# Performance work log

Measured on AMD Instinct MI355X. Metric: run time of the kernel, lower is better.

The kernel has to match this reference:

```python
import jax, jax.numpy as jnp
import numpy as np

CUTOFF = 32.0  # matches init_kwargs cutoff


def _reduce_single(elem, cutoff):
    """elem: [T, D]. Returns (means_padded [T, D], n_segs scalar int32).

    Faithful to the torch loop: representative = elem[0]; walk frames; when
    ||rep - frame|| > cutoff, close the segment [rep_id:f_ind] (mean over it)
    and restart at `frame`. Final open segment is also emitted. Because the
    number of segments is data-dependent, we return a fixed-shape [T, D]
    buffer whose first n_segs rows are the stacked segment means (rest zeros).
    """
    T, D = elem.shape

    def step(rep, frame):
        d = jnp.linalg.norm(rep - frame)  # torch.norm default = Frobenius/L2
        new_seg = d > cutoff
        rep = jnp.where(new_seg, frame, rep)
        return rep, new_seg

    # flags[i] == True means frame i+1 starts a new segment
    _, flags = jax.lax.scan(step, elem[0], elem[1:])
    flags = jnp.concatenate([jnp.zeros((1,), dtype=bool), flags])  # frame 0 never starts anew
    seg_id = jnp.cumsum(flags.astype(jnp.int32))  # [T], ordered segment ids
    n_segs = seg_id[-1] + 1

    sums = jax.ops.segment_sum(elem, seg_id, num_segments=T)  # [T, D]
    counts = jax.ops.segment_sum(jnp.ones((T,), elem.dtype), seg_id, num_segments=T)  # [T]
    means = sums / jnp.maximum(counts, 1.0)[:, None]  # padded rows stay 0
    return means, n_segs


def setup_inputs() -> dict:
    key = jax.random.key(0)
    batch = jax.random.normal(key, (16, 4096, 512), dtype=jnp.float32)
    return {"batch": batch}


def reference(batch):
    # vmap over the list-of-sequences batch dim (all sequences same length T)
    means, n_segs = jax.vmap(lambda e: _reduce_single(e, CUTOFF))(batch)
    return means, n_segs
```

## Files before the change

### kernel.cpp

```cpp
#include <hip/hip_runtime.h>

#define NB 16
#define NT 4096
#define ND 512
#define NLEV 12
#define UPSTRIDE 4104

__global__ __launch_bounds__(256) void kA_next(const float* __restrict__ in,
                                               int* __restrict__ nxt) {
    int lin  = blockIdx.x * 4 + (threadIdx.x >> 6);
    int lane = threadIdx.x & 63;
    int b = lin >> 12;
    int j = lin & (NT - 1);
    const float* base = in + (size_t)b * NT * ND;
    const float4* repp = (const float4*)(base + (size_t)j * ND);
    float4 r0 = repp[lane];
    float4 r1 = repp[lane + 64];
    int i = j + 1;
    for (; i < NT; ++i) {
        const float4* fp = (const float4*)(base + (size_t)i * ND);
        float4 x0 = fp[lane];
        float4 x1 = fp[lane + 64];
        float d0 = r0.x - x0.x, d1 = r0.y - x0.y, d2 = r0.z - x0.z, d3 = r0.w - x0.w;
        float d4 = r1.x - x1.x, d5 = r1.y - x1.y, d6 = r1.z - x1.z, d7 = r1.w - x1.w;
        double s = (double)d0 * d0 + (double)d1 * d1 + (double)d2 * d2 + (double)d3 * d3
                 + (double)d4 * d4 + (double)d5 * d5 + (double)d6 * d6 + (double)d7 * d7;
        #pragma unroll
        for (int off = 32; off >= 1; off >>= 1) s += __shfl_xor(s, off, 64);
        float sf = (float)s;
        if (sqrtf(sf) > 32.0f) break;
    }
    if (lane == 0) nxt[b * NT + j] = i;
}

__global__ __launch_bounds__(256) void kB_build(const int* __restrict__ nxt,
                                                unsigned short* __restrict__ up) {
    __shared__ unsigned short cur[NT + 8];
    __shared__ unsigned short nx[NT + 8];
    int b = blockIdx.x;
    int t = threadIdx.x;
    for (int j = t; j <= NT; j += 256)
        cur[j] = (j < NT) ? (unsigned short)nxt[b * NT + j] : (unsigned short)NT;
    __syncthreads();
    {
        unsigned short* d0 = up + (size_t)(0 * NB + b) * UPSTRIDE;
        for (int j = t; j <= NT; j += 256) d0[j] = cur[j];
    }
    for (int k = 1; k < NLEV; ++k) {
        for (int j = t; j <= NT; j += 256) nx[j] = cur[cur[j]];
        __syncthreads();
        for (int j = t; j <= NT; j += 256) cur[j] = nx[j];
        __syncthreads();
        unsigned short* dk = up + (size_t)(k * NB + b) * UPSTRIDE;
        for (int j = t; j <= NT; j += 256) dk[j] = cur[j];
    }
}

__global__ __launch_bounds__(256) void kC_descend(const unsigned short* __restrict__ up,
                                                  int* __restrict__ start,
                                                  int* __restrict__ nseg,
                                                  float* __restrict__ out_tail) {
    int idx = blockIdx.x * 256 + threadIdx.x;
    int b = idx >> 12;
    int i = idx & (NT - 1);
    int pos = 0, cnt = 0;
    #pragma unroll
    for (int k = NLEV - 1; k >= 0; --k) {
        int t = up[(size_t)(k * NB + b) * UPSTRIDE + pos];
        if (t <= i) { pos = t; cnt += (1 << k); }
    }
    if (pos == i) start[b * NT + cnt] = i;
    if (i == NT - 1) {
        nseg[b] = cnt + 1;
        out_tail[b] = (float)(cnt + 1);
    }
}

__global__ __launch_bounds__(128) void kD_means(const float* __restrict__ in,
                                                const int* __restrict__ nxt,
                                                const int* __restrict__ start,
                                                const int* __restrict__ nseg,
                                                float* __restrict__ out) {
    int r = blockIdx.x & (NT - 1);
    int b = blockIdx.x >> 12;
    int t = threadIdx.x;
    float4 acc = make_float4(0.f, 0.f, 0.f, 0.f);
    int n = nseg[b];
    if (r < n) {
        int s = start[b * NT + r];
        int e = nxt[b * NT + s];
        const float4* base = (const float4*)(in + (size_t)(b * NT + s) * ND);
        int cnt = e - s;
        for (int f = 0; f < cnt; ++f) {
            float4 v = base[(size_t)f * (ND / 4) + t];
            acc.x += v.x; acc.y += v.y; acc.z += v.z; acc.w += v.w;
        }
        float c = (float)cnt;
        acc.x /= c; acc.y /= c; acc.z /= c; acc.w /= c;
    }
    ((float4*)out)[(size_t)(b * NT + r) * (ND / 4) + t] = acc;
}

extern "C" void kernel_launch(void* const* d_in, const int* in_sizes, int n_in,
                              void* d_out, int out_size, void* d_ws, size_t ws_size,
                              hipStream_t stream) {
    const float* in = (const float*)d_in[0];
    float* out = (float*)d_out;
    char* ws = (char*)d_ws;

    int*            nxt   = (int*)(ws + 0);
    int*            start = (int*)(ws + 262144);
    int*            nseg  = (int*)(ws + 524288);
    unsigned short* up    = (unsigned short*)(ws + 524352);

    kA_next   <<<NB * NT / 4,  256, 0, stream>>>(in, nxt);
    kB_build  <<<NB,           256, 0, stream>>>(nxt, up);
    kC_descend<<<NB * NT / 256,256, 0, stream>>>(up, start, nseg,
                                                 out + (size_t)NB * NT * ND);
    kD_means  <<<NB * NT,      128, 0, stream>>>(in, nxt, start, nseg, out);
}
```

Measured before the change: 363.9 us.

## Screen distances in fp32 with exact fallback, unroll scan by four, retile builds

The next-segment search now computes four candidate rows at once using fp32 FMAs and interleaved wave reductions. Only rows whose squared distance falls near the threshold are recomputed with the original double-precision path, which removes most fp64 work and serialized shuffle chains. The pointer-jumping build kernel moves to 1024 threads per block. The means kernel assigns eight output rows per wave with 256-thread blocks, so far fewer blocks are launched. The screening band assumes fp32 error stays below 0.25, which risks mismatches if that bound is violated.

```diff
diff --git a/kernel.cpp b/kernel.cpp
--- a/kernel.cpp
+++ b/kernel.cpp
@@ -5,6 +5,46 @@
 #define ND 512
 #define NLEV 12
 #define UPSTRIDE 4104
+
+#define DIST8_F32(sout, y0, y1)                                   \
+    {                                                             \
+        float d_;                                                 \
+        d_ = r0.x - (y0).x; sout = d_ * d_;                       \
+        d_ = r0.y - (y0).y; sout = fmaf(d_, d_, sout);            \
+        d_ = r0.z - (y0).z; sout = fmaf(d_, d_, sout);            \
+        d_ = r0.w - (y0).w; sout = fmaf(d_, d_, sout);            \
+        d_ = r1.x - (y1).x; sout = fmaf(d_, d_, sout);            \
+        d_ = r1.y - (y1).y; sout = fmaf(d_, d_, sout);            \
+        d_ = r1.z - (y1).z; sout = fmaf(d_, d_, sout);            \
+        d_ = r1.w - (y1).w; sout = fmaf(d_, d_, sout);            \
+    }
+
+__device__ __forceinline__ bool decide_exact(const float* __restrict__ base, int row,
+                                             int lane, float4 r0, float4 r1) {
+    const float4* fp = (const float4*)(base + (size_t)row * ND);
+    float4 y0 = fp[lane];
+    float4 y1 = fp[lane + 64];
+    float d;
+    double sd;
+    d = r0.x - y0.x; sd  = (double)d * d;
+    d = r0.y - y0.y; sd += (double)d * d;
+    d = r0.z - y0.z; sd += (double)d * d;
+    d = r0.w - y0.w; sd += (double)d * d;
+    d = r1.x - y1.x; sd += (double)d * d;
+    d = r1.y - y1.y; sd += (double)d * d;
+    d = r1.z - y1.z; sd += (double)d * d;
+    d = r1.w - y1.w; sd += (double)d * d;
+    #pragma unroll
+    for (int off = 32; off >= 1; off >>= 1) sd += __shfl_xor(sd, off, 64);
+    return ((float)sd > 1024.0f);
+}
+
+__device__ __forceinline__ bool screen1(float sk, const float* __restrict__ base,
+                                        int row, int lane, float4 r0, float4 r1) {
+    if (sk > 1024.25f) return true;
+    if (sk < 1023.75f) return false;
+    return decide_exact(base, row, lane, r0, r1);
+}
 
 __global__ __launch_bounds__(256) void kA_next(const float* __restrict__ in,
                                                int* __restrict__ nxt) {
@@ -16,43 +56,69 @@
     const float4* repp = (const float4*)(base + (size_t)j * ND);
     float4 r0 = repp[lane];
     float4 r1 = repp[lane + 64];
+
+    int result = NT;
     int i = j + 1;
-    for (; i < NT; ++i) {
-        const float4* fp = (const float4*)(base + (size_t)i * ND);
-        float4 x0 = fp[lane];
-        float4 x1 = fp[lane + 64];
-        float d0 = r0.x - x0.x, d1 = r0.y - x0.y, d2 = r0.z - x0.z, d3 = r0.w - x0.w;
-        float d4 = r1.x - x1.x, d5 = r1.y - x1.y, d6 = r1.z - x1.z, d7 = r1.w - x1.w;
-        double s = (double)d0 * d0 + (double)d1 * d1 + (double)d2 * d2 + (double)d3 * d3
-                 + (double)d4 * d4 + (double)d5 * d5 + (double)d6 * d6 + (double)d7 * d7;
+    while (i < NT) {
+        int row0 = i;
+        int row1 = (i + 1 < NT) ? i + 1 : NT - 1;
+        int row2 = (i + 2 < NT) ? i + 2 : NT - 1;
+        int row3 = (i + 3 < NT) ? i + 3 : NT - 1;
+        const float4* f0 = (const float4*)(base + (size_t)row0 * ND);
+        const float4* f1 = (const float4*)(base + (size_t)row1 * ND);
+        const float4* f2 = (const float4*)(base + (size_t)row2 * ND);
+        const float4* f3 = (const float4*)(base + (size_t)row3 * ND);
+        float4 a0 = f0[lane], b0 = f0[lane + 64];
+        float4 a1 = f1[lane], b1 = f1[lane + 64];
+        float4 a2 = f2[lane], b2 = f2[lane + 64];
+        float4 a3 = f3[lane], b3 = f3[lane + 64];
+
+        float s0, s1, s2, s3;
+        DIST8_F32(s0, a0, b0);
+        DIST8_F32(s1, a1, b1);
+        DIST8_F32(s2, a2, b2);
+        DIST8_F32(s3, a3, b3);
+
         #pragma unroll
-        for (int off = 32; off >= 1; off >>= 1) s += __shfl_xor(s, off, 64);
-        float sf = (float)s;
-        if (sqrtf(sf) > 32.0f) break;
+        for (int off = 32; off >= 1; off >>= 1) {
+            s0 += __shfl_xor(s0, off, 64);
+            s1 += __shfl_xor(s1, off, 64);
+            s2 += __shfl_xor(s2, off, 64);
+            s3 += __shfl_xor(s3, off, 64);
+        }
+
+        int nv = NT - i;
+        int found = -1;
+        if (screen1(s0, base, row0, lane, r0, r1)) found = i;
+        else if (nv > 1 && screen1(s1, base, row1, lane, r0, r1)) found = i + 1;
+        else if (nv > 2 && screen1(s2, base, row2, lane, r0, r1)) found = i + 2;
+        else if (nv > 3 && screen1(s3, base, row3, lane, r0, r1)) found = i + 3;
+        if (found >= 0) { result = found; break; }
+        i += 4;
     }
-    if (lane == 0) nxt[b * NT + j] = i;
+    if (lane == 0) nxt[b * NT + j] = result;
 }
 
-__global__ __launch_bounds__(256) void kB_build(const int* __restrict__ nxt,
-                                                unsigned short* __restrict__ up) {
+__global__ __launch_bounds__(1024) void kB_build(const int* __restrict__ nxt,
+                                                 unsigned short* __restrict__ up) {
     __shared__ unsigned short cur[NT + 8];
     __shared__ unsigned short nx[NT + 8];
     int b = blockIdx.x;
     int t = threadIdx.x;
-    for (int j = t; j <= NT; j += 256)
+    for (int j = t; j <= NT; j += 1024)
         cur[j] = (j < NT) ? (unsigned short)nxt[b * NT + j] : (unsigned short)NT;
     __syncthreads();
     {
         unsigned short* d0 = up + (size_t)(0 * NB + b) * UPSTRIDE;
-        for (int j = t; j <= NT; j += 256) d0[j] = cur[j];
+        for (int j = t; j <= NT; j += 1024) d0[j] = cur[j];
     }
     for (int k = 1; k < NLEV; ++k) {
-        for (int j = t; j <= NT; j += 256) nx[j] = cur[cur[j]];
+        for (int j = t; j <= NT; j += 1024) nx[j] = cur[cur[j]];
         __syncthreads();
-        for (int j = t; j <= NT; j += 256) cur[j] = nx[j];
+        for (int j = t; j <= NT; j += 1024) cur[j] = nx[j];
         __syncthreads();
         unsigned short* dk = up + (size_t)(k * NB + b) * UPSTRIDE;
-        for (int j = t; j <= NT; j += 256) dk[j] = cur[j];
+        for (int j = t; j <= NT; j += 1024) dk[j] = cur[j];
     }
 }
 
@@ -76,29 +142,40 @@
     }
 }
 
-__global__ __launch_bounds__(128) void kD_means(const float* __restrict__ in,
+__global__ __launch_bounds__(256) void kD_means(const float* __restrict__ in,
                                                 const int* __restrict__ nxt,
                                                 const int* __restrict__ start,
                                                 const int* __restrict__ nseg,
                                                 float* __restrict__ out) {
-    int r = blockIdx.x & (NT - 1);
-    int b = blockIdx.x >> 12;
-    int t = threadIdx.x;
-    float4 acc = make_float4(0.f, 0.f, 0.f, 0.f);
-    int n = nseg[b];
-    if (r < n) {
-        int s = start[b * NT + r];
-        int e = nxt[b * NT + s];
-        const float4* base = (const float4*)(in + (size_t)(b * NT + s) * ND);
-        int cnt = e - s;
-        for (int f = 0; f < cnt; ++f) {
-            float4 v = base[(size_t)f * (ND / 4) + t];
-            acc.x += v.x; acc.y += v.y; acc.z += v.z; acc.w += v.w;
+    int wid  = threadIdx.x >> 6;
+    int lane = threadIdx.x & 63;
+    int g = blockIdx.x * 4 + wid;
+    int L0 = g * 8;
+    for (int L = L0; L < L0 + 8; ++L) {
+        int b = L >> 12;
+        int r = L & (NT - 1);
+        float4 acc0 = make_float4(0.f, 0.f, 0.f, 0.f);
+        float4 acc1 = make_float4(0.f, 0.f, 0.f, 0.f);
+        int n = nseg[b];
+        if (r < n) {
+            int s = start[b * NT + r];
+            int e = nxt[b * NT + s];
+            const float4* base = (const float4*)(in + (size_t)(b * NT + s) * ND);
+            int cnt = e - s;
+            for (int f = 0; f < cnt; ++f) {
+                float4 v0 = base[(size_t)f * (ND / 4) + lane];
+                float4 v1 = base[(size_t)f * (ND / 4) + lane + 64];
+                acc0.x += v0.x; acc0.y += v0.y; acc0.z += v0.z; acc0.w += v0.w;
+                acc1.x += v1.x; acc1.y += v1.y; acc1.z += v1.z; acc1.w += v1.w;
+            }
+            float c = (float)cnt;
+            acc0.x /= c; acc0.y /= c; acc0.z /= c; acc0.w /= c;
+            acc1.x /= c; acc1.y /= c; acc1.z /= c; acc1.w /= c;
         }
-        float c = (float)cnt;
-        acc.x /= c; acc.y /= c; acc.z /= c; acc.w /= c;
+        float4* orow = (float4*)(out + (size_t)(b * NT + r) * ND);
+        orow[lane]      = acc0;
+        orow[lane + 64] = acc1;
     }
-    ((float4*)out)[(size_t)(b * NT + r) * (ND / 4) + t] = acc;
 }
 
 extern "C" void kernel_launch(void* const* d_in, const int* in_sizes, int n_in,
@@ -113,9 +190,9 @@
     int*            nseg  = (int*)(ws + 524288);
     unsigned short* up    = (unsigned short*)(ws + 524352);
 
-    kA_next   <<<NB * NT / 4,  256, 0, stream>>>(in, nxt);
-    kB_build  <<<NB,           256, 0, stream>>>(nxt, up);
-    kC_descend<<<NB * NT / 256,256, 0, stream>>>(up, start, nseg,
-                                                 out + (size_t)NB * NT * ND);
-    kD_means  <<<NB * NT,      128, 0, stream>>>(in, nxt, start, nseg, out);
+    kA_next   <<<NB * NT / 4,   256,  0, stream>>>(in, nxt);
+    kB_build  <<<NB,            1024, 0, stream>>>(nxt, up);
+    kC_descend<<<NB * NT / 256, 256,  0, stream>>>(up, start, nseg,
+                                                   out + (size_t)NB * NT * ND);
+    kD_means  <<<2048,          256,  0, stream>>>(in, nxt, start, nseg, out);
 }
```

After: 334.7 us. -8.0%, faster.
